# Performance work log

Measured on AMD Instinct MI355X. Metric: run time of the kernel, lower is better.

The kernel has to match this reference:

```python
import jax, jax.numpy as jnp
import numpy as np


def _blur_kernel():
    # make_kernel([1,3,3,1]) -> outer product, normalized; * upsample_factor**2 (=4)
    k = np.array([1.0, 3.0, 3.0, 1.0], dtype=np.float32)
    k2 = np.outer(k, k)
    k2 /= k2.sum()
    k2 *= 4.0
    return jnp.asarray(k2)  # [4,4]


def setup_inputs() -> dict:
    key = jax.random.key(0)
    ks = jax.random.split(key, 6)
    B, Cin, Cout, H, W = 8, 128, 128, 128, 128
    style_dim, sd = 512, 32
    lin_out = Cin * (sd // 2) * (sd // 2)  # 128*16*16 = 32768
    return {
        "x": jax.random.normal(ks[0], (B, Cin, H, W), jnp.float32),
        "style": jax.random.normal(ks[1], (B, style_dim), jnp.float32),
        "weight": jax.random.normal(ks[2], (Cout, Cin, 3, 3), jnp.float32),
        "lin_w": jax.random.normal(ks[3], (lin_out, style_dim), jnp.float32),
        "lin_b": jnp.ones((lin_out,), jnp.float32),  # bias_init=1
        "convw_w": jax.random.normal(ks[4], (Cout, Cin, 3, 3), jnp.float32),
        "convw_b": jnp.zeros((Cout,), jnp.float32),
        "convb_w": jax.random.normal(ks[5], (Cout, Cin, 3, 3), jnp.float32),
        "convb_b": jnp.zeros((Cout,), jnp.float32),
    }


DN = ('NCHW', 'OIHW', 'NCHW')


def reference(x, style, weight, lin_w, lin_b, convw_w, convw_b, convb_w, convb_b):
    B, Cin, H, W = x.shape
    Cout, K = weight.shape[0], weight.shape[2]
    scale = 1.0 / np.sqrt(Cin * K * K)  # equalized-lr scale, fan_in = Cin*K*K
    w = scale * weight  # [Cout, Cin, K, K]; identical per-sample -> plain conv

    # F.conv_transpose2d(stride=2, padding=0) == dilated conv with flipped kernel
    out = jax.lax.conv_general_dilated(
        x, jnp.flip(w, (2, 3)), (1, 1), [(K - 1, K - 1)] * 2,
        lhs_dilation=(2, 2), dimension_numbers=DN)  # [B, Cout, 2H+1, 2W+1]

    # upfirdn2d blur with pad=(1,1): depthwise conv with flipped 4x4 kernel
    bk = _blur_kernel()
    bw = jnp.tile(jnp.flip(bk, (0, 1))[None, None], (Cout, 1, 1, 1))  # [Cout,1,4,4]
    out = jax.lax.conv_general_dilated(
        out, bw, (1, 1), [(1, 1), (1, 1)], feature_group_count=Cout,
        dimension_numbers=DN)  # [B, Cout, 2H, 2W]

    # InstanceNorm2d(affine=False), eps=1e-5, biased variance
    mu = out.mean((2, 3), keepdims=True)
    var = out.var((2, 3), keepdims=True)
    out = (out - mu) * jax.lax.rsqrt(var + 1e-5)
    Ho, Wo = out.shape[2], out.shape[3]

    # spatial_modulation_shared: EqualLinear (fused_lrelu) + View
    half = int(round(np.sqrt(lin_w.shape[0] // Cin)))  # spatial_dim // 2
    sd = 2 * half
    lscale = 1.0 / np.sqrt(style.shape[1])
    s = style @ (lin_w * lscale).T
    s = jax.nn.leaky_relu(s + lin_b, 0.2) * np.sqrt(2.0)  # fused_leaky_relu
    smap = s.reshape(B, Cin, half, half)
    # nn.Upsample(scale_factor=2, mode='nearest')
    smap = jnp.repeat(jnp.repeat(smap, 2, axis=2), 2, axis=3)  # [B,Cin,sd,sd]

    # two EqualConv2d(Cin, Cout, 3, padding=1)
    cscale = 1.0 / np.sqrt(Cin * 9)
    sw = jax.lax.conv_general_dilated(smap, convw_w * cscale, (1, 1),
                                      [(1, 1), (1, 1)], dimension_numbers=DN)
    sw = sw + convw_b[None, :, None, None]
    sb = jax.lax.conv_general_dilated(smap, convb_w * cscale, (1, 1),
                                      [(1, 1), (1, 1)], dimension_numbers=DN)
    sb = sb + convb_b[None, :, None, None]

    # F.interpolate(mode='nearest') to (Ho, Wo)
    hi = jnp.arange(Ho) * sd // Ho
    wi = jnp.arange(Wo) * sd // Wo
    sw = sw[:, :, hi][:, :, :, wi]
    sb = sb[:, :, hi][:, :, :, wi]

    return out * (1.0 + 0.3 * sw) + 0.3 * sb
```

## Files before the change

kernel.cpp:

```cpp
#include <hip/hip_runtime.h>
#include <cstdint>

#define SCALE_MAIN 0.029462782549439483f
#define LSCALE     0.044194173824159223f
#define CSCALE     0.029462782549439483f

typedef __attribute__((ext_vector_type(8))) short bf16x8;
typedef __attribute__((ext_vector_type(4))) float f32x4;
typedef __attribute__((ext_vector_type(2))) unsigned int u32x2;
typedef __attribute__((ext_vector_type(4))) unsigned int u32x4;

static __device__ __forceinline__ float lrelu_s2(float v) {
  return (v > 0.f ? v : 0.2f * v) * 1.4142135623730951f;
}
static __device__ __forceinline__ unsigned short f2bf(float f) {
  unsigned int u = __builtin_bit_cast(unsigned int, f);
  u += 0x7FFFu + ((u >> 16) & 1u);
  return (unsigned short)(u >> 16);
}
static __device__ __forceinline__ float lo16(unsigned int v) {
  return __builtin_bit_cast(float, v << 16);
}
static __device__ __forceinline__ float hi16(unsigned int v) {
  return __builtin_bit_cast(float, v & 0xFFFF0000u);
}
#define EX(arr, rel) (((rel) & 1) ? lo16((arr)[((rel) + 1) >> 1]) : hi16((arr)[((rel) + 1) >> 1]))

__global__ __launch_bounds__(256) void prep_all(
    const float* __restrict__ weight, const float* __restrict__ cw_w,
    const float* __restrict__ cb_w, const float* __restrict__ x,
    const float* __restrict__ style, const float* __restrict__ lin_w,
    const float* __restrict__ lin_b, short* __restrict__ kbu,
    short* __restrict__ kb2, unsigned short* __restrict__ xt,
    unsigned short* __restrict__ smap_bf) {
  int bid = blockIdx.x;
  int t = threadIdx.x;
  if (bid < 2048) {
    int idx = bid * 256 + t;
    int j   = idx & 7;
    int co  = (idx >> 3) & 255;
    int kc  = (idx >> 11) & 63;
    int par = idx >> 17;
    int k = kc * 8 + j;
    int t2 = k >> 7, ci = k & 127;
    int dy2 = t2 >> 1, dx2 = t2 & 1;
    int ph = par >> 1, pw = par & 1;
    const float* wsrc = (co < 128)
        ? cw_w + ((size_t)co * 128 + ci) * 9
        : cb_w + ((size_t)(co - 128) * 128 + ci) * 9;
    float acc = 0.f;
    #pragma unroll
    for (int kh = 0; kh < 3; ++kh) {
      bool okh = dy2 == 0 ? (ph == 0 ? kh == 0 : kh <= 1)
                          : (ph == 0 ? kh >= 1 : kh == 2);
      if (!okh) continue;
      #pragma unroll
      for (int kw = 0; kw < 3; ++kw) {
        bool okw = dx2 == 0 ? (pw == 0 ? kw == 0 : kw <= 1)
                            : (pw == 0 ? kw >= 1 : kw == 2);
        if (okw) acc += wsrc[kh * 3 + kw];
      }
    }
    kb2[idx] = (short)f2bf(acc * CSCALE);
  } else if (bid < 2624) {
    int idx2 = (bid - 2048) * 256 + t;
    int j    = idx2 & 7;
    int co   = (idx2 >> 3) & 127;
    int ksub = (idx2 >> 10) & 3;
    int s    = (idx2 >> 12) & 3;
    int tp   = idx2 >> 14;
    int ci = s * 32 + ksub * 8 + j;
    int wr = (tp == 0 || tp == 1 || tp == 4) ? 2
           : (tp >= 6) ? 1 : 0;
    int wc = (tp == 0 || tp == 2 || tp == 6) ? 2
           : (tp == 4 || tp == 5 || tp == 8) ? 1 : 0;
    float v = weight[((size_t)(co * 128 + ci)) * 9 + wr * 3 + wc] * SCALE_MAIN;
    kbu[idx2] = (short)f2bf(v);
  } else if (bid < 3648) {
    int q = bid - 2624;
    int y = q & 127, b = q >> 7;
    __shared__ unsigned short tl[128 * 134];
    #pragma unroll 4
    for (int i = 0; i < 16; ++i) {
      int c = t + i * 256;
      int ci = c >> 5, x4 = c & 31;
      f32x4 v = *(const f32x4*)(x + (size_t)(b * 128 + ci) * 16384 + y * 128 + x4 * 4);
      unsigned int* dst = (unsigned int*)(tl + ci * 134 + x4 * 4);
      dst[0] = (unsigned int)f2bf(v.x) | ((unsigned int)f2bf(v.y) << 16);
      dst[1] = (unsigned int)f2bf(v.z) | ((unsigned int)f2bf(v.w) << 16);
    }
    __syncthreads();
    #pragma unroll 2
    for (int i = 0; i < 8; ++i) {
      int c = t + i * 256;
      int xcol = c >> 4, sub = c & 15;
      unsigned short u[8];
      #pragma unroll
      for (int j = 0; j < 8; ++j) u[j] = tl[(sub * 8 + j) * 134 + xcol];
      u32x4 o;
      o.x = (unsigned int)u[0] | ((unsigned int)u[1] << 16);
      o.y = (unsigned int)u[2] | ((unsigned int)u[3] << 16);
      o.z = (unsigned int)u[4] | ((unsigned int)u[5] << 16);
      o.w = (unsigned int)u[6] | ((unsigned int)u[7] << 16);
      *(u32x4*)(xt + ((size_t)(b * 128 + y) * 128 + xcol) * 128 + sub * 8) = o;
    }
  } else {
    int wid = t >> 6, lane = t & 63;
    int gw = (bid - 3648) * 4 + wid;
    const float4* st4 = (const float4*)style;
    float s[8][8];
    #pragma unroll
    for (int b = 0; b < 8; ++b) {
      float4 a0 = st4[b * 128 + lane * 2];
      float4 a1 = st4[b * 128 + lane * 2 + 1];
      s[b][0] = a0.x; s[b][1] = a0.y; s[b][2] = a0.z; s[b][3] = a0.w;
      s[b][4] = a1.x; s[b][5] = a1.y; s[b][6] = a1.z; s[b][7] = a1.w;
    }
    for (int rr = 0; rr < 16; ++rr) {
      int j = gw * 16 + rr;
      const float4* wp = (const float4*)(lin_w + (size_t)j * 512);
      float4 w0 = wp[lane * 2], w1 = wp[lane * 2 + 1];
      float acc[8];
      #pragma unroll
      for (int b = 0; b < 8; ++b) {
        acc[b] = w0.x * s[b][0] + w0.y * s[b][1] + w0.z * s[b][2] + w0.w * s[b][3]
               + w1.x * s[b][4] + w1.y * s[b][5] + w1.z * s[b][6] + w1.w * s[b][7];
      }
      #pragma unroll
      for (int m = 32; m; m >>= 1) {
        #pragma unroll
        for (int b = 0; b < 8; ++b) acc[b] += __shfl_xor(acc[b], m, 64);
      }
      if (lane == 0) {
        float bias = lin_b[j];
        int ci = j >> 8, sp = j & 255;
        #pragma unroll
        for (int b = 0; b < 8; ++b)
          smap_bf[(size_t)(b * 256 + sp) * 128 + ci] =
              f2bf(lrelu_s2(acc[b] * LSCALE + bias));
      }
    }
  }
}

__global__ __launch_bounds__(512, 2) void modconv_kernel(
    const unsigned short* __restrict__ smap_bf, const short* __restrict__ kb2,
    const float* __restrict__ cw_b, const float* __restrict__ cb_b,
    float* __restrict__ swp) {
  extern __shared__ __align__(16) char dsm[];
  int par = blockIdx.x, b = blockIdx.y;
  int ph = par >> 1, pw = par & 1;
  int t = threadIdx.x, lane = t & 63, w = t >> 6;
  int q = w >> 1, ch = w & 1;
  int m15 = lane & 15, ksub = lane >> 4;

  for (int c = t; c < 4624; c += 512) {
    int s = c >> 4, cch = c & 15;
    int rr = s / 17, cc = s - rr * 17;
    int gr = rr - 1 + ph, gc = cc - 1 + pw;
    u32x4 v = {0u, 0u, 0u, 0u};
    if ((unsigned)gr < 16u && (unsigned)gc < 16u)
      v = *(const u32x4*)(smap_bf + ((size_t)(b * 256 + gr * 16 + gc) * 128 + cch * 8));
    int phys = (cch + s) & 15;
    *(u32x4*)(dsm + s * 256 + phys * 16) = v;
  }
  __syncthreads();

  const bf16x8* kbv = (const bf16x8*)kb2;
  f32x4 acc[4][8];
  #pragma unroll
  for (int i = 0; i < 4; ++i)
  #pragma unroll
  for (int j = 0; j < 8; ++j) acc[i][j] = (f32x4){0.f, 0.f, 0.f, 0.f};

  for (int s = 0; s < 16; ++s) {
    int t2 = s >> 2, dy2 = t2 >> 1, dx2 = t2 & 1;
    int cch = (s & 3) * 4 + ksub;
    bf16x8 av[4];
    #pragma unroll
    for (int mf = 0; mf < 4; ++mf) {
      int i = q * 4 + mf;
      int ssp = (i + dy2) * 17 + (m15 + dx2);
      int phys = (cch + ssp) & 15;
      av[mf] = *(const bf16x8*)(dsm + ssp * 256 + phys * 16);
    }
    #pragma unroll
    for (int nf = 0; nf < 8; ++nf) {
      bf16x8 bv = kbv[(size_t)((par * 64 + s * 4 + ksub) * 256 + ch * 128 + nf * 16 + m15)];
      #pragma unroll
      for (int mf = 0; mf < 4; ++mf)
        acc[mf][nf] = __builtin_amdgcn_mfma_f32_16x16x32_bf16(av[mf], bv, acc[mf][nf], 0, 0, 0);
    }
  }

  int jbase = ksub * 4;
  #pragma unroll
  for (int nf = 0; nf < 8; ++nf) {
    int co = ch * 128 + nf * 16 + m15;
    float bias = (co < 128) ? cw_b[co] : cb_b[co - 128];
    #pragma unroll
    for (int mf = 0; mf < 4; ++mf) {
      int i = q * 4 + mf;
      #pragma unroll
      for (int r = 0; r < 4; ++r) {
        int px = i * 16 + jbase + r;
        swp[((size_t)(b * 256 + co) * 4 + par) * 256 + px] = acc[mf][nf][r] + bias;
      }
    }
  }
}

__global__ __launch_bounds__(256, 2) void convt_kernel(
    const unsigned short* __restrict__ xt, const short* __restrict__ kbu,
    unsigned short* __restrict__ out1) {
  __shared__ __align__(16) char smem[26112];
  int cg = blockIdx.x, rp = blockIdx.y, b = blockIdx.z;
  int t = threadIdx.x, lane = t & 63, w = t >> 6;
  int m15 = lane & 15, ksub = lane >> 4;
  int pl = (w + cg + rp) & 3;
  int tstart = (pl == 0) ? 0 : 2 + 2 * pl;
  int nst = 16 >> ((pl + 1) >> 1);

  const char* xtc = (const char*)xt;
  for (int c = t; c < 1632; c += 256) {
    int spos = c >> 4, sub = c & 15;
    int lr = spos / 34, lc = spos - lr * 34;
    int y = 2 * rp - 1 + lr, xg = 32 * cg - 1 + lc;
    f32x4 v = {0.f, 0.f, 0.f, 0.f};
    if ((unsigned)y < 128u && (unsigned)xg < 128u)
      v = *(const f32x4*)(xtc + ((size_t)((b * 128 + y) * 128 + xg)) * 256 + sub * 16);
    int phys = (sub & 8) | ((sub ^ spos) & 7);
    *(f32x4*)(smem + spos * 256 + phys * 16) = v;
  }
  __syncthreads();

  const bf16x8* kbv = (const bf16x8*)kbu;
  f32x4 acc[4][8];
  #pragma unroll
  for (int i = 0; i < 4; ++i)
  #pragma unroll
  for (int j = 0; j < 8; ++j) acc[i][j] = (f32x4){0.f, 0.f, 0.f, 0.f};

  auto LD = [&](int s, bf16x8* av, bf16x8* bv) {
    int tap = tstart + (s >> 2);
    int du = -((0x13 >> tap) & 1);
    int dv = -((0x45 >> tap) & 1);
    int cc = s & 3;
    int c = cc * 4 + ksub;
    #pragma unroll
    for (int mf = 0; mf < 4; ++mf) {
      int spos = ((mf >> 1) + du + 1) * 34 + (mf & 1) * 16 + m15 + dv + 1;
      int phys = (c & 8) | ((c ^ spos) & 7);
      av[mf] = *(const bf16x8*)(smem + spos * 256 + phys * 16);
    }
    int bb = tap * 2048 + cc * 512 + ksub * 128 + m15;
    #pragma unroll
    for (int nf = 0; nf < 8; ++nf) bv[nf] = kbv[bb + nf * 16];
  };
  auto MM = [&](bf16x8* av, bf16x8* bv) {
    __builtin_amdgcn_s_setprio(1);
    #pragma unroll
    for (int nf = 0; nf < 8; ++nf)
    #pragma unroll
    for (int mf = 0; mf < 4; ++mf)
      acc[mf][nf] = __builtin_amdgcn_mfma_f32_16x16x32_bf16(av[mf], bv[nf], acc[mf][nf], 0, 0, 0);
    __builtin_amdgcn_s_setprio(0);
  };

  bf16x8 aA[4], bA[8], aB[4], bB[8];
  LD(0, aA, bA);
  for (int s = 0; s + 2 <= nst; s += 2) {
    LD(s + 1, aB, bB);
    MM(aA, bA);
    if (s + 2 < nst) LD(s + 2, aA, bA);
    MM(aB, bB);
  }

  __syncthreads();
  float* eps = (float*)smem;
  int t63 = t & 63, wpl = t >> 6;
  #pragma unroll
  for (int nf = 0; nf < 8; ++nf) {
    #pragma unroll
    for (int mf = 0; mf < 4; ++mf)
    #pragma unroll
    for (int r = 0; r < 4; ++r)
      eps[(pl * 64 + mf * 16 + ksub * 4 + r) * 17 + m15] = acc[mf][nf][r];
    __syncthreads();
    #pragma unroll
    for (int k = 0; k < 4; ++k) {
      int slot = k * 64 + t63;
      int co16 = slot >> 4, pr = (slot >> 3) & 1, ch = slot & 7;
      float v0 = eps[(wpl * 64 + pr * 32 + ch * 4 + 0) * 17 + co16];
      float v1 = eps[(wpl * 64 + pr * 32 + ch * 4 + 1) * 17 + co16];
      float v2 = eps[(wpl * 64 + pr * 32 + ch * 4 + 2) * 17 + co16];
      float v3 = eps[(wpl * 64 + pr * 32 + ch * 4 + 3) * 17 + co16];
      u32x2 o;
      o.x = (unsigned int)f2bf(v0) | ((unsigned int)f2bf(v1) << 16);
      o.y = (unsigned int)f2bf(v2) | ((unsigned int)f2bf(v3) << 16);
      int co = nf * 16 + co16;
      int r = 2 * rp + pr;
      size_t ob = (((size_t)(b * 4 + wpl) * 128 + co) * 130 + r) * 132
                + 32 * cg + ch * 4;
      if (cg < 4 || ch == 0) *(u32x2*)(out1 + ob) = o;
    }
    __syncthreads();
  }
}

template <int PASS>
__global__ __launch_bounds__(256) void blur_kernel(
    const unsigned short* __restrict__ out1, float* __restrict__ part,
    const float* __restrict__ swp, float* __restrict__ dout) {
  __shared__ unsigned short S[18][4][144];
  __shared__ float lsw[4][32], lsb[4][32];
  __shared__ float msh[2];
  __shared__ float rb2[8];
  int g = blockIdx.x, co = blockIdx.y, b = blockIdx.z;
  int t = threadIdx.x, lane = t & 63, wid = t >> 6;
  int bc = b * 128 + co;

  if (PASS == 1) {
    if (t == 0) {
      float a1 = 0.f, a2 = 0.f;
      #pragma unroll
      for (int i = 0; i < 8; ++i) {
        a1 += part[((size_t)bc * 8 + i) * 2];
        a2 += part[((size_t)bc * 8 + i) * 2 + 1];
      }
      float mean = a1 * (1.f / 65536.f);
      float var = a2 * (1.f / 65536.f) - mean * mean;
      msh[0] = mean; msh[1] = rsqrtf(var + 1e-5f);
    }
    {
      int which = t >> 7;
      int par = (t >> 5) & 3;
      int idx = t & 31;
      int hrow = idx >> 4, wcol = idx & 15;
      int px2 = (2 * g + hrow) * 16 + wcol;
      float v = swp[((size_t)(b * 256 + which * 128 + co) * 4 + par) * 256 + px2];
      if (which == 0) lsw[par][idx] = v; else lsb[par][idx] = v;
    }
  }

  int rbase = 16 * g - 1;
  for (int i = t; i < 1152; i += 256) {
    int rid = i >> 4, ch = i & 15;
    int lr = rid >> 2, pl = rid & 3;
    int r = rbase + lr;
    u32x2 v0 = {0u, 0u}, v1 = {0u, 0u};
    if (r >= 0) {
      const unsigned short* src =
          out1 + ((size_t)((b * 4 + pl) * 128 + co) * 130 + r) * 132 + ch * 8;
      v0 = *(const u32x2*)(src);
      v1 = *(const u32x2*)(src + 4);
    }
    *(u32x2*)(&S[lr][pl][8 + ch * 8]) = v0;
    *(u32x2*)(&S[lr][pl][12 + ch * 8]) = v1;
  }
  if (t < 72) {
    int lr = t >> 2, pl = t & 3;
    int r = rbase + lr;
    u32x2 v = {0u, 0u};
    if (r >= 0)
      v = *(const u32x2*)(out1 + ((size_t)((b * 4 + pl) * 128 + co) * 130 + r) * 132 + 128);
    *(u32x2*)(&S[lr][pl][136]) = v;
  }
  if (t >= 128 && t < 200) {
    int q = t - 128;
    *(unsigned int*)(&S[q >> 2][q & 3][6]) = 0u;
  }
  __syncthreads();

  float mean = 0.f, rstd = 0.f;
  if (PASS == 1) { mean = msh[0]; rstd = msh[1]; }

  int rg = t >> 5, cg = t & 31;
  int sr = 2 * rg;
  unsigned int Eu[2][3][4], Ou[2][4][4];
  #pragma unroll
  for (int cp = 0; cp < 2; ++cp) {
    #pragma unroll
    for (int rr = 0; rr < 3; ++rr) {
      const unsigned int* p = (const unsigned int*)&S[sr + 1 + rr][cp][0];
      #pragma unroll
      for (int j = 0; j < 4; ++j) Eu[cp][rr][j] = p[2 * cg + 3 + j];
    }
    #pragma unroll
    for (int rr = 0; rr < 4; ++rr) {
      const unsigned int* p = (const unsigned int*)&S[sr + rr][2 + cp][0];
      #pragma unroll
      for (int j = 0; j < 4; ++j) Ou[cp][rr][j] = p[2 * cg + 3 + j];
    }
  }

  float s1 = 0.f, s2 = 0.f;
  #pragma unroll
  for (int k = 0; k < 4; ++k) {
    const int a = (k + 1) >> 1;
    float Tc[2][6];
    #pragma unroll
    for (int cp = 0; cp < 2; ++cp)
    #pragma unroll
    for (int rel = 0; rel < 6; ++rel) {
      float v;
      if ((k & 1) == 0)
        v = EX(Ou[cp][a], rel) + 3.f * EX(Eu[cp][a], rel)
          + 3.f * EX(Ou[cp][a + 1], rel) + EX(Eu[cp][a + 1], rel);
      else
        v = EX(Eu[cp][a - 1], rel) + 3.f * EX(Ou[cp][a], rel)
          + 3.f * EX(Eu[cp][a], rel) + EX(Ou[cp][a + 1], rel);
      Tc[cp][rel] = v;
    }
    float o8[8];
    #pragma unroll
    for (int i = 0; i < 4; ++i) {
      float ve = ((Tc[1][i] + Tc[0][i + 2]) + 3.f * (Tc[0][i + 1] + Tc[1][i + 1])) * 0.0625f;
      float vo = ((Tc[0][i + 1] + Tc[1][i + 2]) + 3.f * (Tc[1][i + 1] + Tc[0][i + 2])) * 0.0625f;
      if (PASS == 0) {
        s1 += ve + vo; s2 += ve * ve + vo * vo;
      } else {
        o8[2 * i] = ve; o8[2 * i + 1] = vo;
      }
    }
    if (PASS == 1) {
      int hl = 4 * rg + k;
      int h = 32 * g + hl;
      int par = ((hl >> 3) & 1) * 2 + (cg & 1);
      int lidx = ((hl >> 4) & 1) * 16 + (cg >> 1);
      float f1 = (1.f + 0.3f * lsw[par][lidx]) * rstd;
      float f0 = 0.3f * lsb[par][lidx] - mean * f1;
      f32x4 oA = {o8[0] * f1 + f0, o8[1] * f1 + f0, o8[2] * f1 + f0, o8[3] * f1 + f0};
      f32x4 oB = {o8[4] * f1 + f0, o8[5] * f1 + f0, o8[6] * f1 + f0, o8[7] * f1 + f0};
      float* op = dout + ((size_t)bc * 256 + h) * 256 + 8 * cg;
      *(f32x4*)(op) = oA;
      *(f32x4*)(op + 4) = oB;
    }
  }

  if (PASS == 0) {
    #pragma unroll
    for (int m = 32; m; m >>= 1) { s1 += __shfl_xor(s1, m, 64); s2 += __shfl_xor(s2, m, 64); }
    if (lane == 0) { rb2[wid * 2] = s1; rb2[wid * 2 + 1] = s2; }
    __syncthreads();
    if (t == 0) {
      part[((size_t)bc * 8 + g) * 2]     = rb2[0] + rb2[2] + rb2[4] + rb2[6];
      part[((size_t)bc * 8 + g) * 2 + 1] = rb2[1] + rb2[3] + rb2[5] + rb2[7];
    }
  }
}

extern "C" void kernel_launch(void* const* d_in, const int* in_sizes, int n_in,
                              void* d_out, int out_size, void* d_ws, size_t ws_size,
                              hipStream_t stream) {
  const float* x      = (const float*)d_in[0];
  const float* style  = (const float*)d_in[1];
  const float* weight = (const float*)d_in[2];
  const float* lin_w  = (const float*)d_in[3];
  const float* lin_b  = (const float*)d_in[4];
  const float* cw_w   = (const float*)d_in[5];
  const float* cw_b   = (const float*)d_in[6];
  const float* cb_w   = (const float*)d_in[7];
  const float* cb_b   = (const float*)d_in[8];
  float* out = (float*)d_out;
  char* ws = (char*)d_ws;

  short*          kbu     = (short*)(ws);
  short*          kb2     = (short*)(ws + 294912);
  unsigned short* xt      = (unsigned short*)(ws + 1343488);
  unsigned short* smap_bf = (unsigned short*)(ws + 34897920);
  float*          swp     = (float*)(ws + 35422208);
  float*          part    = (float*)(ws + 43810816);
  unsigned short* out1    = (unsigned short*)(ws + 43941888);

  prep_all<<<dim3(4160), dim3(256), 0, stream>>>(
      weight, cw_w, cb_w, x, style, lin_w, lin_b, kbu, kb2, xt, smap_bf);
  modconv_kernel<<<dim3(4, 8), dim3(512), 73984, stream>>>(smap_bf, kb2, cw_b, cb_b, swp);
  convt_kernel<<<dim3(5, 65, 8), dim3(256), 0, stream>>>(xt, kbu, out1);
  blur_kernel<0><<<dim3(8, 128, 8), dim3(256), 0, stream>>>(out1, part, swp, out);
  blur_kernel<1><<<dim3(8, 128, 8), dim3(256), 0, stream>>>(out1, part, swp, out);
}
```

Before: 343.8 us.

## Store blurred bf16 intermediate and apply instance norm in separate elementwise pass

Replaces the two-pass blur (compute stats, then recompute the blur and normalize) with a single blur pass that writes the blurred result as bf16 along with partial stats, a tiny stats reduction kernel, and a streaming elementwise normalize/modulate kernel. This avoids recomputing the blur and rereading out1 with halos a second time, at the cost of an extra 32MB bf16 intermediate write and read. It is gated on the workspace being large enough, and otherwise falls back to the old path.

```diff
diff --git a/kernel.cpp b/kernel.cpp
--- a/kernel.cpp
+++ b/kernel.cpp
@@ -308,6 +308,152 @@
   }
 }
 
+__global__ __launch_bounds__(256) void blurstats_kernel(
+    const unsigned short* __restrict__ out1, float* __restrict__ part,
+    unsigned short* __restrict__ blurred) {
+  __shared__ unsigned short S[18][4][144];
+  __shared__ float rb2[8];
+  int g = blockIdx.x, co = blockIdx.y, b = blockIdx.z;
+  int t = threadIdx.x, lane = t & 63, wid = t >> 6;
+  int bc = b * 128 + co;
+
+  int rbase = 16 * g - 1;
+  for (int i = t; i < 1152; i += 256) {
+    int rid = i >> 4, ch = i & 15;
+    int lr = rid >> 2, pl = rid & 3;
+    int r = rbase + lr;
+    u32x2 v0 = {0u, 0u}, v1 = {0u, 0u};
+    if (r >= 0) {
+      const unsigned short* src =
+          out1 + ((size_t)((b * 4 + pl) * 128 + co) * 130 + r) * 132 + ch * 8;
+      v0 = *(const u32x2*)(src);
+      v1 = *(const u32x2*)(src + 4);
+    }
+    *(u32x2*)(&S[lr][pl][8 + ch * 8]) = v0;
+    *(u32x2*)(&S[lr][pl][12 + ch * 8]) = v1;
+  }
+  if (t < 72) {
+    int lr = t >> 2, pl = t & 3;
+    int r = rbase + lr;
+    u32x2 v = {0u, 0u};
+    if (r >= 0)
+      v = *(const u32x2*)(out1 + ((size_t)((b * 4 + pl) * 128 + co) * 130 + r) * 132 + 128);
+    *(u32x2*)(&S[lr][pl][136]) = v;
+  }
+  if (t >= 128 && t < 200) {
+    int q = t - 128;
+    *(unsigned int*)(&S[q >> 2][q & 3][6]) = 0u;
+  }
+  __syncthreads();
+
+  int rg = t >> 5, cg = t & 31;
+  int sr = 2 * rg;
+  unsigned int Eu[2][3][4], Ou[2][4][4];
+  #pragma unroll
+  for (int cp = 0; cp < 2; ++cp) {
+    #pragma unroll
+    for (int rr = 0; rr < 3; ++rr) {
+      const unsigned int* p = (const unsigned int*)&S[sr + 1 + rr][cp][0];
+      #pragma unroll
+      for (int j = 0; j < 4; ++j) Eu[cp][rr][j] = p[2 * cg + 3 + j];
+    }
+    #pragma unroll
+    for (int rr = 0; rr < 4; ++rr) {
+      const unsigned int* p = (const unsigned int*)&S[sr + rr][2 + cp][0];
+      #pragma unroll
+      for (int j = 0; j < 4; ++j) Ou[cp][rr][j] = p[2 * cg + 3 + j];
+    }
+  }
+
+  float s1 = 0.f, s2 = 0.f;
+  #pragma unroll
+  for (int k = 0; k < 4; ++k) {
+    const int a = (k + 1) >> 1;
+    float Tc[2][6];
+    #pragma unroll
+    for (int cp = 0; cp < 2; ++cp)
+    #pragma unroll
+    for (int rel = 0; rel < 6; ++rel) {
+      float v;
+      if ((k & 1) == 0)
+        v = EX(Ou[cp][a], rel) + 3.f * EX(Eu[cp][a], rel)
+          + 3.f * EX(Ou[cp][a + 1], rel) + EX(Eu[cp][a + 1], rel);
+      else
+        v = EX(Eu[cp][a - 1], rel) + 3.f * EX(Ou[cp][a], rel)
+          + 3.f * EX(Eu[cp][a], rel) + EX(Ou[cp][a + 1], rel);
+      Tc[cp][rel] = v;
+    }
+    float o8[8];
+    #pragma unroll
+    for (int i = 0; i < 4; ++i) {
+      float ve = ((Tc[1][i] + Tc[0][i + 2]) + 3.f * (Tc[0][i + 1] + Tc[1][i + 1])) * 0.0625f;
+      float vo = ((Tc[0][i + 1] + Tc[1][i + 2]) + 3.f * (Tc[1][i + 1] + Tc[0][i + 2])) * 0.0625f;
+      s1 += ve + vo; s2 += ve * ve + vo * vo;
+      o8[2 * i] = ve; o8[2 * i + 1] = vo;
+    }
+    int h = 32 * g + 4 * rg + k;
+    u32x4 o;
+    o.x = (unsigned int)f2bf(o8[0]) | ((unsigned int)f2bf(o8[1]) << 16);
+    o.y = (unsigned int)f2bf(o8[2]) | ((unsigned int)f2bf(o8[3]) << 16);
+    o.z = (unsigned int)f2bf(o8[4]) | ((unsigned int)f2bf(o8[5]) << 16);
+    o.w = (unsigned int)f2bf(o8[6]) | ((unsigned int)f2bf(o8[7]) << 16);
+    *(u32x4*)(blurred + ((size_t)bc * 256 + h) * 256 + 8 * cg) = o;
+  }
+
+  #pragma unroll
+  for (int m = 32; m; m >>= 1) { s1 += __shfl_xor(s1, m, 64); s2 += __shfl_xor(s2, m, 64); }
+  if (lane == 0) { rb2[wid * 2] = s1; rb2[wid * 2 + 1] = s2; }
+  __syncthreads();
+  if (t == 0) {
+    part[((size_t)bc * 8 + g) * 2]     = rb2[0] + rb2[2] + rb2[4] + rb2[6];
+    part[((size_t)bc * 8 + g) * 2 + 1] = rb2[1] + rb2[3] + rb2[5] + rb2[7];
+  }
+}
+
+__global__ __launch_bounds__(256) void stats_kernel(const float* __restrict__ part,
+                                                    float* __restrict__ stats) {
+  int bc = blockIdx.x * 256 + threadIdx.x;
+  float s1 = 0.f, s2 = 0.f;
+  #pragma unroll
+  for (int i = 0; i < 8; ++i) {
+    s1 += part[((size_t)bc * 8 + i) * 2];
+    s2 += part[((size_t)bc * 8 + i) * 2 + 1];
+  }
+  float mean = s1 * (1.f / 65536.f);
+  float var = s2 * (1.f / 65536.f) - mean * mean;
+  stats[bc * 2] = mean;
+  stats[bc * 2 + 1] = rsqrtf(var + 1e-5f);
+}
+
+__global__ __launch_bounds__(256) void final_elem(
+    const unsigned short* __restrict__ blurred, const float* __restrict__ swp,
+    const float* __restrict__ stats, float* __restrict__ dout) {
+  unsigned int tid = blockIdx.x * 256 + threadIdx.x;
+  unsigned int e = tid * 8;
+  unsigned int w = e & 255u;
+  unsigned int h = (e >> 8) & 255u;
+  unsigned int bc = e >> 16;
+  unsigned int b = bc >> 7, co = bc & 127u;
+  float mean = stats[bc * 2], rstd = stats[bc * 2 + 1];
+  unsigned int par = ((h >> 3) & 1u) * 2 + ((w >> 3) & 1u);
+  unsigned int px2 = (h >> 4) * 16 + (w >> 4);
+  float msw = swp[((size_t)(b * 256 + co) * 4 + par) * 256 + px2];
+  float msb = swp[((size_t)(b * 256 + 128 + co) * 4 + par) * 256 + px2];
+  float f1 = (1.f + 0.3f * msw) * rstd;
+  float f0 = 0.3f * msb - mean * f1;
+  u32x4 uv = *(const u32x4*)(blurred + e);
+  float o[8];
+  #pragma unroll
+  for (int j = 0; j < 4; ++j) {
+    unsigned int word = uv[j];
+    o[2 * j]     = lo16(word) * f1 + f0;
+    o[2 * j + 1] = hi16(word) * f1 + f0;
+  }
+  f32x4 a = {o[0], o[1], o[2], o[3]}, c = {o[4], o[5], o[6], o[7]};
+  *(f32x4*)(dout + e) = a;
+  *(f32x4*)(dout + e + 4) = c;
+}
+
 template <int PASS>
 __global__ __launch_bounds__(256) void blur_kernel(
     const unsigned short* __restrict__ out1, float* __restrict__ part,
@@ -471,12 +617,21 @@
   unsigned short* smap_bf = (unsigned short*)(ws + 34897920);
   float*          swp     = (float*)(ws + 35422208);
   float*          part    = (float*)(ws + 43810816);
+  float*          stats   = (float*)(ws + 43941888 - 8192);
   unsigned short* out1    = (unsigned short*)(ws + 43941888);
+  unsigned short* blurred = (unsigned short*)(ws + 184516608);
+  bool huge = ws_size >= (size_t)318734336;
 
   prep_all<<<dim3(4160), dim3(256), 0, stream>>>(
       weight, cw_w, cb_w, x, style, lin_w, lin_b, kbu, kb2, xt, smap_bf);
   modconv_kernel<<<dim3(4, 8), dim3(512), 73984, stream>>>(smap_bf, kb2, cw_b, cb_b, swp);
   convt_kernel<<<dim3(5, 65, 8), dim3(256), 0, stream>>>(xt, kbu, out1);
-  blur_kernel<0><<<dim3(8, 128, 8), dim3(256), 0, stream>>>(out1, part, swp, out);
-  blur_kernel<1><<<dim3(8, 128, 8), dim3(256), 0, stream>>>(out1, part, swp, out);
-}
+  if (huge) {
+    blurstats_kernel<<<dim3(8, 128, 8), dim3(256), 0, stream>>>(out1, part, blurred);
+    stats_kernel<<<dim3(4), dim3(256), 0, stream>>>(part, stats);
+    final_elem<<<dim3(32768), dim3(256), 0, stream>>>(blurred, swp, stats, out);
+  } else {
+    blur_kernel<0><<<dim3(8, 128, 8), dim3(256), 0, stream>>>(out1, part, swp, out);
+    blur_kernel<1><<<dim3(8, 128, 8), dim3(256), 0, stream>>>(out1, part, swp, out);
+  }
+}
```

Result: slower. 354.0 us (+3.0%).
